# Kernel tuning notes

Hardware: AMD Instinct MI355X
Metric: run time of the kernel (lower is better)

## Reference

```python
import jax, jax.numpy as jnp
import numpy as np
import math

HIDDEN = 1024
N_HEADS = 16
HEAD = HIDDEN // N_HEADS

def setup_inputs() -> dict:
    key = jax.random.key(0)
    k1, k2, k3 = jax.random.split(key, 3)
    encodings = jax.random.normal(k1, (2, 2048, HIDDEN), dtype=jnp.float32)
    W_attn = jax.random.normal(k2, (HIDDEN, 3 * HIDDEN), dtype=jnp.float32) * 0.02
    b_attn = jnp.zeros((3 * HIDDEN,), dtype=jnp.float32)
    W_out = jax.random.normal(k3, (HIDDEN, HIDDEN), dtype=jnp.float32) * 0.02
    b_out = jnp.zeros((HIDDEN,), dtype=jnp.float32)
    return {"encodings": encodings, "W_attn": W_attn, "b_attn": b_attn,
            "W_out": W_out, "b_out": b_out}

def reference(encodings, W_attn, b_attn, W_out, b_out):
    b, n, _ = encodings.shape
    qkv = encodings @ W_attn + b_attn              # [b, n, 3*hidden]
    q, k, v = jnp.split(qkv, 3, axis=-1)
    # 'b n (h l) -> b h n l'
    def to_heads(t):
        return t.reshape(b, n, N_HEADS, HEAD).transpose(0, 2, 1, 3)
    q, k, v = to_heads(q), to_heads(k), to_heads(v)
    # scores[b,h,k,q]; causal mask keeps key_pos <= query_pos
    scores = jnp.einsum('bhki,bhqi->bhkq', k, q) / math.sqrt(HEAD)
    mask = jnp.arange(n)[:, None] <= jnp.arange(n)[None, :]   # [k, q]
    scores = jnp.where(mask, scores, jnp.float32(-10000.0))
    attn = jax.nn.softmax(scores, axis=2)          # softmax over key dim
    combined = jnp.einsum('bhkq,bhkl->bhql', attn, v)  # [b, h, n, head]
    out = combined.transpose(0, 2, 1, 3).reshape(b, n, HIDDEN)
    return out @ W_out + b_out
```

## Files before the change

### kernel.cpp

```cpp
#include <hip/hip_runtime.h>
#include <hip/hip_bf16.h>

typedef __attribute__((ext_vector_type(8))) short bf16x8;
typedef __attribute__((ext_vector_type(4))) short bf16x4;
typedef __attribute__((ext_vector_type(4))) float f32x4;

__device__ __forceinline__ short f2bf(float f) {
    unsigned u = __float_as_uint(f);
    u += 0x7fff + ((u >> 16) & 1);
    return (short)(u >> 16);
}
__device__ __forceinline__ float bf2f(short s) {
    return __uint_as_float(((unsigned)(unsigned short)s) << 16);
}
__device__ __forceinline__ unsigned pk_bf16(float lo, float hi) {
    __hip_bfloat162 t = __float22bfloat162_rn(make_float2(lo, hi));
    unsigned u;
    __builtin_memcpy(&u, &t, 4);
    return u;
}

#define GLOAD_LDS16(gp, lp)                                                            \
    __builtin_amdgcn_global_load_lds(                                                  \
        (const __attribute__((address_space(1))) unsigned*)(gp),                       \
        (__attribute__((address_space(3))) unsigned*)(lp), 16, 0, 0)

#define QK_SCALE 0.180336879f
#define MFMA16(a, b, c) __builtin_amdgcn_mfma_f32_16x16x32_bf16((a), (b), (c), 0, 0, 0)

__device__ __forceinline__ void tcvt_tile(const float* __restrict__ W, short* __restrict__ Wt,
                                          int K, int N, int bx, int by, int t,
                                          short (*tile)[72]) {
    const int k0 = by * 64, n0 = bx * 64;
    #pragma unroll
    for (int jj = 0; jj < 4; ++jj) {
        int row = jj * 16 + (t >> 4);
        int col = (t & 15) * 4;
        f32x4 v = *(const f32x4*)&W[(size_t)(k0 + row) * N + n0 + col];
        bf16x4 b = {f2bf(v.x), f2bf(v.y), f2bf(v.z), f2bf(v.w)};
        *(bf16x4*)&tile[row][col] = b;
    }
    __syncthreads();
    const int nr = t >> 2, kc = (t & 3) * 16;
    bf16x8 o0, o1;
    #pragma unroll
    for (int j = 0; j < 8; ++j) { o0[j] = tile[kc + j][nr]; o1[j] = tile[kc + 8 + j][nr]; }
    short* dst = &Wt[(size_t)(n0 + nr) * K + k0 + kc];
    *(bf16x8*)dst = o0;
    *(bf16x8*)(dst + 8) = o1;
}

__global__ __launch_bounds__(256) void prep_kernel(
    const float* __restrict__ enc, const float* __restrict__ Wa,
    const float* __restrict__ ba, const float* __restrict__ Wo,
    const float* __restrict__ bo, short* __restrict__ Abf,
    short* __restrict__ WtA, short* __restrict__ bbA,
    short* __restrict__ WtO, short* __restrict__ bbO)
{
    __shared__ alignas(16) short tile[64][72];
    const int id = blockIdx.x, t = threadIdx.x;
    if (id < 2048) {
        const int i = id * 2048 + t * 8;
        f32x4 a = *(const f32x4*)&enc[i];
        f32x4 b = *(const f32x4*)&enc[i + 4];
        bf16x8 o = {f2bf(a.x), f2bf(a.y), f2bf(a.z), f2bf(a.w),
                    f2bf(b.x), f2bf(b.y), f2bf(b.z), f2bf(b.w)};
        *(bf16x8*)&Abf[i] = o;
    } else if (id == 2048) {
        for (int j = t * 8; j < 3072; j += 2048) {
            f32x4 a = *(const f32x4*)&ba[j];
            f32x4 b = *(const f32x4*)&ba[j + 4];
            bf16x8 o = {f2bf(a.x), f2bf(a.y), f2bf(a.z), f2bf(a.w),
                        f2bf(b.x), f2bf(b.y), f2bf(b.z), f2bf(b.w)};
            *(bf16x8*)&bbA[j] = o;
        }
    } else if (id == 2049) {
        if (t < 128) {
            const int j = t * 8;
            f32x4 a = *(const f32x4*)&bo[j];
            f32x4 b = *(const f32x4*)&bo[j + 4];
            bf16x8 o = {f2bf(a.x), f2bf(a.y), f2bf(a.z), f2bf(a.w),
                        f2bf(b.x), f2bf(b.y), f2bf(b.z), f2bf(b.w)};
            *(bf16x8*)&bbO[j] = o;
        }
        __syncthreads();
    } else if (id < 2818) {
        const int lid = id - 2050;
        tcvt_tile(Wa, WtA, 1024, 3072, lid % 48, lid / 48, t, tile);
    } else {
        const int lid = id - 2818;
        tcvt_tile(Wo, WtO, 1024, 1024, lid % 16, lid / 16, t, tile);
    }
}

template<int BN, bool F32OUT, bool SPLIT3>
__global__ __launch_bounds__(256) void gemm_bt(
    const short* __restrict__ A, const short* __restrict__ Bt,
    const short* __restrict__ bias, void* __restrict__ C,
    short* __restrict__ Kw, short* __restrict__ Vw, int M, int N, int K)
{
    __shared__ alignas(16) short As[128 * 32];
    __shared__ alignas(16) short Bs[BN * 32];

    const int tid = threadIdx.x, w = tid >> 6, lane = tid & 63;
    const int quad = lane >> 4, l16 = lane & 15;
    constexpr int MT = (BN == 128) ? 4 : 2;
    const int wm = (BN == 128) ? (w >> 1) : w;
    const int wn = (BN == 128) ? (w & 1) : 0;
    const int m0 = blockIdx.y * 128, n0 = blockIdx.x * BN;
    const int srow = lane >> 2, scol = (lane & 3) * 8;

    f32x4 acc[MT][4] = {};

    for (int k0 = 0; k0 < K; k0 += 32) {
        __syncthreads();
        #pragma unroll
        for (int jj = 0; jj < 2; ++jj) {
            const int rb = w * 32 + jj * 16;
            GLOAD_LDS16(&A[(size_t)(m0 + rb + srow) * K + k0 + scol], &As[rb * 32]);
        }
        if (BN == 128) {
            #pragma unroll
            for (int jj = 0; jj < 2; ++jj) {
                const int rb = w * 32 + jj * 16;
                GLOAD_LDS16(&Bt[(size_t)(n0 + rb + srow) * K + k0 + scol], &Bs[rb * 32]);
            }
        } else {
            const int rb = w * 16;
            GLOAD_LDS16(&Bt[(size_t)(n0 + rb + srow) * K + k0 + scol], &Bs[rb * 32]);
        }
        __syncthreads();
        bf16x8 af[MT], bfr[4];
        #pragma unroll
        for (int i = 0; i < MT; ++i)
            af[i] = *(const bf16x8*)&As[(wm * (MT * 16) + i * 16 + l16) * 32 + quad * 8];
        #pragma unroll
        for (int i = 0; i < 4; ++i)
            bfr[i] = *(const bf16x8*)&Bs[(wn * 64 + i * 16 + l16) * 32 + quad * 8];
        #pragma unroll
        for (int mt = 0; mt < MT; ++mt)
            #pragma unroll
            for (int nt = 0; nt < 4; ++nt)
                acc[mt][nt] = MFMA16(af[mt], bfr[nt], acc[mt][nt]);
    }

    if (SPLIT3) {
        const int g = n0 >> 10;
        short* dstb = (g == 0) ? (short*)C : (g == 1) ? Kw : Vw;
        const int lc0 = n0 & 1023;
        #pragma unroll
        for (int nt = 0; nt < 4; ++nt) {
            const int col = n0 + wn * 64 + nt * 16 + l16;
            const int lc = lc0 + wn * 64 + nt * 16 + l16;
            const float bv = bf2f(bias[col]);
            #pragma unroll
            for (int mt = 0; mt < 4; ++mt) {
                const int row = m0 + wm * 64 + mt * 16 + quad * 4;
                #pragma unroll
                for (int r = 0; r < 4; ++r) {
                    float v = acc[mt][nt][r] + bv;
                    if (g == 0) v *= QK_SCALE;
                    dstb[(size_t)(row + r) * 1024 + lc] = f2bf(v);
                }
            }
        }
    } else {
        #pragma unroll
        for (int nt = 0; nt < 4; ++nt) {
            const int col = n0 + wn * 64 + nt * 16 + l16;
            const float bv = bf2f(bias[col]);
            #pragma unroll
            for (int mt = 0; mt < MT; ++mt) {
                const int row = m0 + wm * (MT * 16) + mt * 16 + quad * 4;
                #pragma unroll
                for (int r = 0; r < 4; ++r) {
                    float v = acc[mt][nt][r] + bv;
                    if (F32OUT) ((float*)C)[(size_t)(row + r) * N + col] = v;
                    else        ((short*)C)[(size_t)(row + r) * N + col] = f2bf(v);
                }
            }
        }
    }
}

__global__ __launch_bounds__(256) void fragprep_kernel(
    const short* __restrict__ Kw, const short* __restrict__ Vw,
    short* __restrict__ Kx, short* __restrict__ Vx)
{
    __shared__ alignas(16) short T[64][72];
    const int t = threadIdx.x;
    const int kc = blockIdx.x, bh = blockIdx.y;
    const int batch = bh >> 4, head = bh & 15;
    const size_t srcbase = ((size_t)batch * 2048 + kc * 64) * 1024 + head * 64;
    short* kxdst = Kx + ((size_t)bh * 32 + kc) * 4096;
    short* vxdst = Vx + ((size_t)bh * 32 + kc) * 4096;

    #pragma unroll
    for (int i = 0; i < 2; ++i) {
        const int c = i * 256 + t;
        const int lane = c & 63, sh = c >> 6;
        const int s = sh >> 1, h = sh & 1;
        const int l16 = lane & 15, quad = lane >> 4;
        bf16x8 v = *(const bf16x8*)&Kw[srcbase + (size_t)(s * 16 + l16) * 1024 + h * 32 + quad * 8];
        *(bf16x8*)&kxdst[c * 8] = v;
    }
    #pragma unroll
    for (int i = 0; i < 2; ++i) {
        const int c = i * 256 + t;
        const int row = c >> 3, d0 = (c & 7) * 8;
        bf16x8 v = *(const bf16x8*)&Vw[srcbase + (size_t)row * 1024 + d0];
        #pragma unroll
        for (int j = 0; j < 8; ++j) T[d0 + j][row] = v[j];
    }
    __syncthreads();
    #pragma unroll
    for (int i = 0; i < 2; ++i) {
        const int c = i * 256 + t;
        const int lane = c & 63, hd = c >> 6;
        const int h = hd >> 2, dt = hd & 3;
        const int l16 = lane & 15, quad = lane >> 4;
        bf16x8 v = *(const bf16x8*)&T[dt * 16 + l16][h * 32 + quad * 8];
        *(bf16x8*)&vxdst[c * 8] = v;
    }
}

__global__ __launch_bounds__(128) void attn_kernel(
    const short* __restrict__ Qw, const short* __restrict__ Kx,
    const short* __restrict__ Vx, short* __restrict__ comb)
{
    __shared__ alignas(16) short Ps[2][2][16 * 72];

    const int tid = threadIdx.x, w = tid >> 6, lane = tid & 63;
    const int quad = lane >> 4, l16 = lane & 15;
    const int bh = blockIdx.x;
    const int tA = blockIdx.y, tB = 63 - tA;
    const int batch = bh >> 4, head = bh & 15;
    const size_t rowbase = (size_t)batch * 2048;
    const int hcol = head * 64;
    const int q0A = tA * 32 + w * 16, q0B = tB * 32 + w * 16;
    const int diagA = tA >> 1, diagB = tB >> 1;
    const short* Kxbh = Kx + (size_t)bh * 131072;
    const short* Vxbh = Vx + (size_t)bh * 131072;
    const int lofs = lane * 8;
    short* pwA = &Ps[w][0][0];
    short* pwB = &Ps[w][1][0];

    bf16x8 qfA[2], qfB[2];
    {
        const short* pa = &Qw[(rowbase + q0A + l16) * 1024 + hcol];
        const short* pb = &Qw[(rowbase + q0B + l16) * 1024 + hcol];
        qfA[0] = *(const bf16x8*)(pa + quad * 8);
        qfA[1] = *(const bf16x8*)(pa + 32 + quad * 8);
        qfB[0] = *(const bf16x8*)(pb + quad * 8);
        qfB[1] = *(const bf16x8*)(pb + 32 + quad * 8);
    }

    f32x4 otA[4] = {}, otB[4] = {};
    float laccA = 0.f, laccB = 0.f;

    bf16x8 kf[4][2];
    #pragma unroll
    for (int s = 0; s < 4; ++s) {
        kf[s][0] = *(const bf16x8*)&Kxbh[(s * 2 + 0) * 512 + lofs];
        kf[s][1] = *(const bf16x8*)&Kxbh[(s * 2 + 1) * 512 + lofs];
    }

    for (int kc = 0; kc <= diagB; ++kc) {
        const bool actA = (kc <= diagA);
        const int key0 = kc * 64;

        const short* vb = Vxbh + kc * 4096;
        bf16x8 vf[2][4];
        #pragma unroll
        for (int h = 0; h < 2; ++h)
            #pragma unroll
            for (int dt = 0; dt < 4; ++dt)
                vf[h][dt] = *(const bf16x8*)&vb[(h * 4 + dt) * 512 + lofs];

        f32x4 svA[4], svB[4];
        #pragma unroll
        for (int s = 0; s < 4; ++s) {
            f32x4 a = {0.f, 0.f, 0.f, 0.f};
            a = MFMA16(kf[s][0], qfB[0], a);
            a = MFMA16(kf[s][1], qfB[1], a);
            svB[s] = a;
            if (actA) {
                f32x4 b = {0.f, 0.f, 0.f, 0.f};
                b = MFMA16(kf[s][0], qfA[0], b);
                b = MFMA16(kf[s][1], qfA[1], b);
                svA[s] = b;
            }
        }

        if (kc < diagB) {
            const short* kb = Kxbh + (kc + 1) * 4096;
            #pragma unroll
            for (int s = 0; s < 4; ++s) {
                kf[s][0] = *(const bf16x8*)&kb[(s * 2 + 0) * 512 + lofs];
                kf[s][1] = *(const bf16x8*)&kb[(s * 2 + 1) * 512 + lofs];
            }
        }

        if (kc == diagB) {
            const int qq = q0B + l16;
            #pragma unroll
            for (int s = 0; s < 4; ++s) {
                const int keyb = key0 + s * 16 + quad * 4;
                #pragma unroll
                for (int r = 0; r < 4; ++r)
                    svB[s][r] = (keyb + r <= qq) ? svB[s][r] : -1e30f;
            }
        }
        #pragma unroll
        for (int s = 0; s < 4; ++s) {
            #pragma unroll
            for (int r = 0; r < 4; ++r) svB[s][r] = exp2f(svB[s][r]);
            laccB += (svB[s][0] + svB[s][1]) + (svB[s][2] + svB[s][3]);
            *(unsigned*)&pwB[l16 * 72 + s * 16 + quad * 4]     = pk_bf16(svB[s][0], svB[s][1]);
            *(unsigned*)&pwB[l16 * 72 + s * 16 + quad * 4 + 2] = pk_bf16(svB[s][2], svB[s][3]);
        }
        if (actA) {
            if (kc == diagA) {
                const int qq = q0A + l16;
                #pragma unroll
                for (int s = 0; s < 4; ++s) {
                    const int keyb = key0 + s * 16 + quad * 4;
                    #pragma unroll
                    for (int r = 0; r < 4; ++r)
                        svA[s][r] = (keyb + r <= qq) ? svA[s][r] : -1e30f;
                }
            }
            #pragma unroll
            for (int s = 0; s < 4; ++s) {
                #pragma unroll
                for (int r = 0; r < 4; ++r) svA[s][r] = exp2f(svA[s][r]);
                laccA += (svA[s][0] + svA[s][1]) + (svA[s][2] + svA[s][3]);
                *(unsigned*)&pwA[l16 * 72 + s * 16 + quad * 4]     = pk_bf16(svA[s][0], svA[s][1]);
                *(unsigned*)&pwA[l16 * 72 + s * 16 + quad * 4 + 2] = pk_bf16(svA[s][2], svA[s][3]);
            }
        }

        {
            bf16x8 pfB0 = *(const bf16x8*)&pwB[l16 * 72 + quad * 8];
            bf16x8 pfB1 = *(const bf16x8*)&pwB[l16 * 72 + 32 + quad * 8];
            #pragma unroll
            for (int dt = 0; dt < 4; ++dt) {
                otB[dt] = MFMA16(vf[0][dt], pfB0, otB[dt]);
                otB[dt] = MFMA16(vf[1][dt], pfB1, otB[dt]);
            }
            if (actA) {
                bf16x8 pfA0 = *(const bf16x8*)&pwA[l16 * 72 + quad * 8];
                bf16x8 pfA1 = *(const bf16x8*)&pwA[l16 * 72 + 32 + quad * 8];
                #pragma unroll
                for (int dt = 0; dt < 4; ++dt) {
                    otA[dt] = MFMA16(vf[0][dt], pfA0, otA[dt]);
                    otA[dt] = MFMA16(vf[1][dt], pfA1, otA[dt]);
                }
            }
        }
    }

    laccA += __shfl_xor(laccA, 16);
    laccA += __shfl_xor(laccA, 32);
    laccB += __shfl_xor(laccB, 16);
    laccB += __shfl_xor(laccB, 32);
    const float invA = 1.0f / laccA, invB = 1.0f / laccB;

    #pragma unroll
    for (int dt = 0; dt < 4; ++dt) {
        *(unsigned*)&pwA[l16 * 72 + dt * 16 + quad * 4]     = pk_bf16(otA[dt][0] * invA, otA[dt][1] * invA);
        *(unsigned*)&pwA[l16 * 72 + dt * 16 + quad * 4 + 2] = pk_bf16(otA[dt][2] * invA, otA[dt][3] * invA);
        *(unsigned*)&pwB[l16 * 72 + dt * 16 + quad * 4]     = pk_bf16(otB[dt][0] * invB, otB[dt][1] * invB);
        *(unsigned*)&pwB[l16 * 72 + dt * 16 + quad * 4 + 2] = pk_bf16(otB[dt][2] * invB, otB[dt][3] * invB);
    }
    {
        const int qr = lane >> 2, dc = (lane & 3) * 16;
        bf16x8 a0 = *(const bf16x8*)&pwA[qr * 72 + dc];
        bf16x8 a1 = *(const bf16x8*)&pwA[qr * 72 + dc + 8];
        short* dstA = &comb[(rowbase + q0A + qr) * 1024 + hcol + dc];
        *(bf16x8*)dstA = a0;
        *(bf16x8*)(dstA + 8) = a1;
        bf16x8 b0 = *(const bf16x8*)&pwB[qr * 72 + dc];
        bf16x8 b1 = *(const bf16x8*)&pwB[qr * 72 + dc + 8];
        short* dstB = &comb[(rowbase + q0B + qr) * 1024 + hcol + dc];
        *(bf16x8*)dstB = b0;
        *(bf16x8*)(dstB + 8) = b1;
    }
}

extern "C" void kernel_launch(void* const* d_in, const int* in_sizes, int n_in,
                              void* d_out, int out_size, void* d_ws, size_t ws_size,
                              hipStream_t stream)
{
    const float* enc = (const float*)d_in[0];
    const float* Wa  = (const float*)d_in[1];
    const float* ba  = (const float*)d_in[2];
    const float* Wo  = (const float*)d_in[3];
    const float* bo  = (const float*)d_in[4];
    float* out = (float*)d_out;

    char* ws = (char*)d_ws;
    short* Abf  = (short*)ws;
    short* Kx   = (short*)ws;
    short* WtO  = (short*)(ws + ((size_t)8 << 20));
    short* bbA  = (short*)(ws + ((size_t)10 << 20));
    short* bbO  = (short*)(ws + ((size_t)10 << 20) + 16384);
    short* WtA  = (short*)(ws + ((size_t)11 << 20));
    short* Vx   = (short*)(ws + ((size_t)11 << 20));
    short* Qw   = (short*)(ws + ((size_t)19 << 20));
    short* Kw   = (short*)(ws + ((size_t)27 << 20));
    short* comb = (short*)(ws + ((size_t)27 << 20));
    short* Vw   = (short*)(ws + ((size_t)35 << 20));

    prep_kernel<<<3074, 256, 0, stream>>>(enc, Wa, ba, Wo, bo, Abf, WtA, bbA, WtO, bbO);
    gemm_bt<128, false, true><<<dim3(24, 32), 256, 0, stream>>>(
        Abf, WtA, bbA, Qw, Kw, Vw, 4096, 3072, 1024);
    fragprep_kernel<<<dim3(32, 32), 256, 0, stream>>>(Kw, Vw, Kx, Vx);
    attn_kernel<<<dim3(32, 32), 128, 0, stream>>>(Qw, Kx, Vx, comb);
    gemm_bt<64, true, false><<<dim3(16, 32), 256, 0, stream>>>(
        comb, WtO, bbO, out, nullptr, nullptr, 4096, 1024, 1024);
}
```

Baseline: 190.2 us.

## Fuse K/V fragment reordering into QKV GEMM epilogue, drop fragprep kernel

The QKV GEMM epilogue now writes K and V directly in the MFMA-fragment layouts the attention kernel consumes, with V stored transposed as packed 4-element vectors. This removes the separate fragprep kernel launch and its extra round-trip of K/V through global memory. The workspace layout is reshuffled to match. The attention kernel also merges pairs of 32-bit LDS stores into single 64-bit stores. The cost is scattered, less coalesced global writes in the GEMM epilogue.

```diff
diff --git a/kernel.cpp b/kernel.cpp
--- a/kernel.cpp
+++ b/kernel.cpp
@@ -97,7 +97,7 @@
 __global__ __launch_bounds__(256) void gemm_bt(
     const short* __restrict__ A, const short* __restrict__ Bt,
     const short* __restrict__ bias, void* __restrict__ C,
-    short* __restrict__ Kw, short* __restrict__ Vw, int M, int N, int K)
+    short* __restrict__ Kx, short* __restrict__ Vx, int M, int N, int K)
 {
     __shared__ alignas(16) short As[128 * 32];
     __shared__ alignas(16) short Bs[BN * 32];
@@ -146,21 +146,59 @@
 
     if (SPLIT3) {
         const int g = n0 >> 10;
-        short* dstb = (g == 0) ? (short*)C : (g == 1) ? Kw : Vw;
-        const int lc0 = n0 & 1023;
-        #pragma unroll
-        for (int nt = 0; nt < 4; ++nt) {
-            const int col = n0 + wn * 64 + nt * 16 + l16;
-            const int lc = lc0 + wn * 64 + nt * 16 + l16;
-            const float bv = bf2f(bias[col]);
-            #pragma unroll
-            for (int mt = 0; mt < 4; ++mt) {
-                const int row = m0 + wm * 64 + mt * 16 + quad * 4;
-                #pragma unroll
-                for (int r = 0; r < 4; ++r) {
-                    float v = acc[mt][nt][r] + bv;
-                    if (g == 0) v *= QK_SCALE;
-                    dstb[(size_t)(row + r) * 1024 + lc] = f2bf(v);
+        if (g == 0) {
+            short* qw = (short*)C;
+            #pragma unroll
+            for (int nt = 0; nt < 4; ++nt) {
+                const int col = n0 + wn * 64 + nt * 16 + l16;
+                const int lc = col & 1023;
+                const float bv = bf2f(bias[col]);
+                #pragma unroll
+                for (int mt = 0; mt < 4; ++mt) {
+                    const int row = m0 + wm * 64 + mt * 16 + quad * 4;
+                    #pragma unroll
+                    for (int r = 0; r < 4; ++r)
+                        qw[(size_t)(row + r) * 1024 + lc] = f2bf((acc[mt][nt][r] + bv) * QK_SCALE);
+                }
+            }
+        } else if (g == 1) {
+            #pragma unroll
+            for (int nt = 0; nt < 4; ++nt) {
+                const int col = n0 + wn * 64 + nt * 16 + l16;
+                const int lc = col & 1023, head = lc >> 6, d = lc & 63;
+                const int h = d >> 5, qk = (d & 31) >> 3, j = d & 7;
+                const float bv = bf2f(bias[col]);
+                #pragma unroll
+                for (int mt = 0; mt < 4; ++mt) {
+                    const int rowA = m0 + wm * 64 + mt * 16 + quad * 4;
+                    const int batch = rowA >> 11, seq = rowA & 2047, kc = seq >> 6;
+                    const int bh = batch * 16 + head;
+                    short* base = &Kx[((size_t)bh * 32 + kc) * 4096
+                                      + ((mt * 2 + h) * 64 + qk * 16 + quad * 4) * 8 + j];
+                    #pragma unroll
+                    for (int r = 0; r < 4; ++r)
+                        base[r * 8] = f2bf(acc[mt][nt][r] + bv);
+                }
+            }
+        } else {
+            #pragma unroll
+            for (int nt = 0; nt < 4; ++nt) {
+                const int col = n0 + wn * 64 + nt * 16 + l16;
+                const int lc = col & 1023, head = lc >> 6, d = lc & 63;
+                const int dt = d >> 4, l16v = d & 15;
+                const float bv = bf2f(bias[col]);
+                #pragma unroll
+                for (int mt = 0; mt < 4; ++mt) {
+                    const int rowA = m0 + wm * 64 + mt * 16 + quad * 4;
+                    const int batch = rowA >> 11, seq = rowA & 2047, kc = seq >> 6;
+                    const int s64 = seq & 63;
+                    const int h = s64 >> 5, q2 = (s64 & 31) >> 3, j0 = s64 & 7;
+                    const int bh = batch * 16 + head;
+                    bf16x4 pk;
+                    #pragma unroll
+                    for (int r = 0; r < 4; ++r) pk[r] = f2bf(acc[mt][nt][r] + bv);
+                    *(bf16x4*)&Vx[((size_t)bh * 32 + kc) * 4096
+                                  + ((h * 4 + dt) * 64 + q2 * 16 + l16v) * 8 + j0] = pk;
                 }
             }
         }
@@ -180,47 +218,6 @@
                 }
             }
         }
-    }
-}
-
-__global__ __launch_bounds__(256) void fragprep_kernel(
-    const short* __restrict__ Kw, const short* __restrict__ Vw,
-    short* __restrict__ Kx, short* __restrict__ Vx)
-{
-    __shared__ alignas(16) short T[64][72];
-    const int t = threadIdx.x;
-    const int kc = blockIdx.x, bh = blockIdx.y;
-    const int batch = bh >> 4, head = bh & 15;
-    const size_t srcbase = ((size_t)batch * 2048 + kc * 64) * 1024 + head * 64;
-    short* kxdst = Kx + ((size_t)bh * 32 + kc) * 4096;
-    short* vxdst = Vx + ((size_t)bh * 32 + kc) * 4096;
-
-    #pragma unroll
-    for (int i = 0; i < 2; ++i) {
-        const int c = i * 256 + t;
-        const int lane = c & 63, sh = c >> 6;
-        const int s = sh >> 1, h = sh & 1;
-        const int l16 = lane & 15, quad = lane >> 4;
-        bf16x8 v = *(const bf16x8*)&Kw[srcbase + (size_t)(s * 16 + l16) * 1024 + h * 32 + quad * 8];
-        *(bf16x8*)&kxdst[c * 8] = v;
-    }
-    #pragma unroll
-    for (int i = 0; i < 2; ++i) {
-        const int c = i * 256 + t;
-        const int row = c >> 3, d0 = (c & 7) * 8;
-        bf16x8 v = *(const bf16x8*)&Vw[srcbase + (size_t)row * 1024 + d0];
-        #pragma unroll
-        for (int j = 0; j < 8; ++j) T[d0 + j][row] = v[j];
-    }
-    __syncthreads();
-    #pragma unroll
-    for (int i = 0; i < 2; ++i) {
-        const int c = i * 256 + t;
-        const int lane = c & 63, hd = c >> 6;
-        const int h = hd >> 2, dt = hd & 3;
-        const int l16 = lane & 15, quad = lane >> 4;
-        bf16x8 v = *(const bf16x8*)&T[dt * 16 + l16][h * 32 + quad * 8];
-        *(bf16x8*)&vxdst[c * 8] = v;
     }
 }
 
@@ -316,8 +313,8 @@
             #pragma unroll
             for (int r = 0; r < 4; ++r) svB[s][r] = exp2f(svB[s][r]);
             laccB += (svB[s][0] + svB[s][1]) + (svB[s][2] + svB[s][3]);
-            *(unsigned*)&pwB[l16 * 72 + s * 16 + quad * 4]     = pk_bf16(svB[s][0], svB[s][1]);
-            *(unsigned*)&pwB[l16 * 72 + s * 16 + quad * 4 + 2] = pk_bf16(svB[s][2], svB[s][3]);
+            uint2 pk = {pk_bf16(svB[s][0], svB[s][1]), pk_bf16(svB[s][2], svB[s][3])};
+            *(uint2*)&pwB[l16 * 72 + s * 16 + quad * 4] = pk;
         }
         if (actA) {
             if (kc == diagA) {
@@ -335,8 +332,8 @@
                 #pragma unroll
                 for (int r = 0; r < 4; ++r) svA[s][r] = exp2f(svA[s][r]);
                 laccA += (svA[s][0] + svA[s][1]) + (svA[s][2] + svA[s][3]);
-                *(unsigned*)&pwA[l16 * 72 + s * 16 + quad * 4]     = pk_bf16(svA[s][0], svA[s][1]);
-                *(unsigned*)&pwA[l16 * 72 + s * 16 + quad * 4 + 2] = pk_bf16(svA[s][2], svA[s][3]);
+                uint2 pk = {pk_bf16(svA[s][0], svA[s][1]), pk_bf16(svA[s][2], svA[s][3])};
+                *(uint2*)&pwA[l16 * 72 + s * 16 + quad * 4] = pk;
             }
         }
 
@@ -368,10 +365,12 @@
 
     #pragma unroll
     for (int dt = 0; dt < 4; ++dt) {
-        *(unsigned*)&pwA[l16 * 72 + dt * 16 + quad * 4]     = pk_bf16(otA[dt][0] * invA, otA[dt][1] * invA);
-        *(unsigned*)&pwA[l16 * 72 + dt * 16 + quad * 4 + 2] = pk_bf16(otA[dt][2] * invA, otA[dt][3] * invA);
-        *(unsigned*)&pwB[l16 * 72 + dt * 16 + quad * 4]     = pk_bf16(otB[dt][0] * invB, otB[dt][1] * invB);
-        *(unsigned*)&pwB[l16 * 72 + dt * 16 + quad * 4 + 2] = pk_bf16(otB[dt][2] * invB, otB[dt][3] * invB);
+        uint2 pa = {pk_bf16(otA[dt][0] * invA, otA[dt][1] * invA),
+                    pk_bf16(otA[dt][2] * invA, otA[dt][3] * invA)};
+        *(uint2*)&pwA[l16 * 72 + dt * 16 + quad * 4] = pa;
+        uint2 pb = {pk_bf16(otB[dt][0] * invB, otB[dt][1] * invB),
+                    pk_bf16(otB[dt][2] * invB, otB[dt][3] * invB)};
+        *(uint2*)&pwB[l16 * 72 + dt * 16 + quad * 4] = pb;
     }
     {
         const int qr = lane >> 2, dc = (lane & 3) * 16;
@@ -401,21 +400,18 @@
 
     char* ws = (char*)d_ws;
     short* Abf  = (short*)ws;
-    short* Kx   = (short*)ws;
+    short* comb = (short*)ws;
     short* WtO  = (short*)(ws + ((size_t)8 << 20));
     short* bbA  = (short*)(ws + ((size_t)10 << 20));
     short* bbO  = (short*)(ws + ((size_t)10 << 20) + 16384);
     short* WtA  = (short*)(ws + ((size_t)11 << 20));
-    short* Vx   = (short*)(ws + ((size_t)11 << 20));
-    short* Qw   = (short*)(ws + ((size_t)19 << 20));
-    short* Kw   = (short*)(ws + ((size_t)27 << 20));
-    short* comb = (short*)(ws + ((size_t)27 << 20));
-    short* Vw   = (short*)(ws + ((size_t)35 << 20));
+    short* Kx   = (short*)(ws + ((size_t)17 << 20));
+    short* Vx   = (short*)(ws + ((size_t)25 << 20));
+    short* Qw   = (short*)(ws + ((size_t)33 << 20));
 
     prep_kernel<<<3074, 256, 0, stream>>>(enc, Wa, ba, Wo, bo, Abf, WtA, bbA, WtO, bbO);
     gemm_bt<128, false, true><<<dim3(24, 32), 256, 0, stream>>>(
-        Abf, WtA, bbA, Qw, Kw, Vw, 4096, 3072, 1024);
-    fragprep_kernel<<<dim3(32, 32), 256, 0, stream>>>(Kw, Vw, Kx, Vx);
+        Abf, WtA, bbA, Qw, Kx, Vx, 4096, 3072, 1024);
     attn_kernel<<<dim3(32, 32), 128, 0, stream>>>(Qw, Kx, Vx, comb);
     gemm_bt<64, true, false><<<dim3(16, 32), 256, 0, stream>>>(
         comb, WtO, bbO, out, nullptr, nullptr, 4096, 1024, 1024);
```

Result: slower. 198.7 us (+4.5%).
